# Kernel optimization log

Hardware: AMD Instinct MI355X
Metric: run time of the kernel (lower is better)

## Reference

```python
import jax, jax.numpy as jnp
import numpy as np

B, N = 256, 4096
IMG_W, IMG_H = 640.0, 480.0


def setup_inputs() -> dict:
    key = jax.random.key(0)
    k0, k1, k2, k3 = jax.random.split(key, 4)
    kpts0 = jax.random.uniform(k0, (B, N, 2), dtype=jnp.float32) * jnp.array([IMG_W, IMG_H], jnp.float32)
    kpts1 = jax.random.uniform(k1, (B, N, 2), dtype=jnp.float32) * jnp.array([IMG_W, IMG_H], jnp.float32)
    conf = jax.random.uniform(k2, (B, N, 1), dtype=jnp.float32)
    t_scale = jax.random.uniform(k3, (B, 2), dtype=jnp.float32) + 0.5
    Kmat = jnp.array([[500.0, 0.0, 320.0], [0.0, 500.0, 240.0], [0.0, 0.0, 1.0]], jnp.float32)
    K = jnp.tile(Kmat[None, None], (B, 2, 1, 1))
    gt_pose_0to1 = jnp.tile(jnp.eye(4, dtype=jnp.float32)[None], (B, 1, 1))
    return {"kpts0": kpts0, "kpts1": kpts1, "conf": conf, "t_scale": t_scale, "K": K, "gt_pose_0to1": gt_pose_0to1}


def _normalize(kpts, Kmat):
    # pixel -> normalized camera coords, homogeneous. kpts:[B,N,2], Kmat:[B,3,3] -> [B,N,3]
    Kinv = jnp.linalg.inv(Kmat)
    h = jnp.concatenate([kpts, jnp.ones_like(kpts[..., :1])], axis=-1)
    return jnp.einsum('bij,bnj->bni', Kinv, h)


def _se3_weighted_8pt(kpts0, kpts1, K0, K1, w, t_scale):
    b_, n_ = kpts0.shape[0], kpts0.shape[1]
    x0 = _normalize(kpts0, K0)  # [B,N,3]
    x1 = _normalize(kpts1, K1)  # [B,N,3]
    # epipolar constraint x1^T E x0 = 0 -> row kron(x1, x0): [B,N,9]
    X = (x1[..., :, None] * x0[..., None, :]).reshape(b_, n_, 9)
    # confidence-weighted normal equations, 9x9 per batch
    M = jnp.einsum('bn,bni,bnj->bij', w, X, X)
    _, V = jnp.linalg.eigh(M)
    E = V[..., 0].reshape(b_, 3, 3)  # eigvec of smallest eigenvalue
    # project to essential manifold + decompose
    U, S, Vt = jnp.linalg.svd(E)
    W = jnp.array([[0.0, -1.0, 0.0], [1.0, 0.0, 0.0], [0.0, 0.0, 1.0]], E.dtype)
    R1 = U @ W @ Vt
    R2 = U @ W.T @ Vt
    R1 = R1 * jnp.sign(jnp.linalg.det(R1))[:, None, None]
    R2 = R2 * jnp.sign(jnp.linalg.det(R2))[:, None, None]
    t = U[..., 2]  # [B,3]
    Rc = jnp.stack([R1, R1, R2, R2], axis=1)   # [B,4,3,3]
    tc = jnp.stack([t, -t, t, -t], axis=1)     # [B,4,3]
    # cheirality: solve d0 * (R x0) - d1 * x1 = -t in least squares (2x2 closed form)
    a = jnp.einsum('bcij,bnj->bcni', Rc, x0)   # [B,4,N,3]
    bvec = x1[:, None]                          # [B,1,N,3]
    tt = tc[:, :, None, :]                      # [B,4,1,3]
    aa = jnp.sum(a * a, -1)
    bb = jnp.sum(bvec * bvec, -1)
    ab = jnp.sum(a * bvec, -1)
    at = jnp.sum(a * tt, -1)
    bt = jnp.sum(bvec * tt, -1)
    det = aa * bb - ab * ab + 1e-9
    d0 = (-at * bb + ab * bt) / det
    d1 = (aa * bt - ab * at) / det
    pos = ((d0 > 0) & (d1 > 0)).astype(w.dtype)
    score = jnp.sum(w[:, None] * pos, -1)       # [B,4]
    best = jnp.argmax(jax.lax.stop_gradient(score), axis=-1)
    oh = jax.nn.one_hot(best, 4, dtype=kpts0.dtype)
    R = jnp.einsum('bc,bcij->bij', oh, Rc)
    t_best = jnp.einsum('bc,bci->bi', oh, tc)
    t_sc = t_best * t_scale[:, None]            # scale unit translation
    top = jnp.concatenate([R, t_sc[..., None]], axis=-1)  # [B,3,4]
    bot = jnp.broadcast_to(jnp.array([0.0, 0.0, 0.0, 1.0], R.dtype), (b_, 1, 4))
    return jnp.concatenate([top, bot], axis=1)  # [B,4,4]


def _se3_inverse(T):
    R = T[:, :3, :3]
    t = T[:, :3, 3:]
    Rt = jnp.swapaxes(R, -1, -2)
    tin = -(Rt @ t)
    top = jnp.concatenate([Rt, tin], axis=-1)
    bot = jnp.broadcast_to(jnp.array([0.0, 0.0, 0.0, 1.0], T.dtype), (T.shape[0], 1, 4))
    return jnp.concatenate([top, bot], axis=1)


def reference(kpts0, kpts1, conf, t_scale, K, gt_pose_0to1):
    w = conf[..., 0]
    T01 = _se3_weighted_8pt(kpts0, kpts1, K[:, 0], K[:, 1], w, t_scale[:, 0])
    T10 = _se3_inverse(T01)
    return jnp.stack([T01, T10], axis=1)  # [B,2,4,4]
```

## Files before the change

kernel.cpp:

```cpp
#include <hip/hip_runtime.h>
#include <math.h>

#define NBATCH 256
#define NPTS   4096

__device__ __forceinline__ void inv3x3d(const float* __restrict__ Km, double* Ki) {
  double a = Km[0], bb = Km[1], c = Km[2];
  double d = Km[3], e  = Km[4], f = Km[5];
  double g = Km[6], h  = Km[7], i = Km[8];
  double C00 =  e*i - f*h;
  double C01 = -(d*i - f*g);
  double C02 =  d*h - e*g;
  double det = a*C00 + bb*C01 + c*C02;
  double rd = 1.0/det;
  Ki[0] = C00*rd; Ki[1] = -(bb*i - c*h)*rd; Ki[2] =  (bb*f - c*e)*rd;
  Ki[3] = C01*rd; Ki[4] =  (a*i  - c*g)*rd; Ki[5] = -(a*f  - c*d)*rd;
  Ki[6] = C02*rd; Ki[7] = -(a*h - bb*g)*rd; Ki[8] =  (a*e  - bb*d)*rd;
}

#define IDX(r,c)   ((r)*((r)+1)/2+(c))
#define UPIDX(r,c) ((r)*9 - ((r)*((r)-1))/2 + ((c)-(r)))

#define K1_T   512
#define K1_PPT (NPTS / K1_T)

__global__ __launch_bounds__(K1_T, 2)
void k1_reduce(const float* __restrict__ kpts0,
               const float* __restrict__ kpts1,
               const float* __restrict__ conf,
               const float* __restrict__ Kmat,
               double* __restrict__ Mws)
{
  const int b    = blockIdx.x;
  const int tid  = threadIdx.x;
  const int lane = tid & 63;
  const int wv   = tid >> 6;

  __shared__ double red[K1_T/64][45];

  double Kd[9];
  float Ki0[9], Ki1[9];
  inv3x3d(Kmat + (size_t)b*18, Kd);
#pragma unroll
  for (int j=0;j<9;j++) Ki0[j] = (float)Kd[j];
  inv3x3d(Kmat + (size_t)b*18 + 9, Kd);
#pragma unroll
  for (int j=0;j<9;j++) Ki1[j] = (float)Kd[j];

  const float2* k0p = (const float2*)kpts0 + (size_t)b*NPTS;
  const float2* k1p = (const float2*)kpts1 + (size_t)b*NPTS;
  const float*  cp  = conf + (size_t)b*NPTS;

  float acc[45];
#pragma unroll
  for (int j=0;j<45;j++) acc[j] = 0.f;

  for (int p=0;p<K1_PPT;p++) {
    const int i = tid + p*K1_T;
    const float2 q0 = k0p[i];
    const float2 q1 = k1p[i];
    const float  w  = cp[i];
    float x0[3], x1[3];
    x0[0] = fmaf(Ki0[0],q0.x, fmaf(Ki0[1],q0.y, Ki0[2]));
    x0[1] = fmaf(Ki0[3],q0.x, fmaf(Ki0[4],q0.y, Ki0[5]));
    x0[2] = fmaf(Ki0[6],q0.x, fmaf(Ki0[7],q0.y, Ki0[8]));
    x1[0] = fmaf(Ki1[0],q1.x, fmaf(Ki1[1],q1.y, Ki1[2]));
    x1[1] = fmaf(Ki1[3],q1.x, fmaf(Ki1[4],q1.y, Ki1[5]));
    x1[2] = fmaf(Ki1[6],q1.x, fmaf(Ki1[7],q1.y, Ki1[8]));
    float X[9], wX[9];
#pragma unroll
    for (int ii=0; ii<3; ii++)
#pragma unroll
      for (int jj=0; jj<3; jj++)
        X[ii*3+jj] = x1[ii]*x0[jj];
#pragma unroll
    for (int j=0;j<9;j++) wX[j] = w*X[j];
    int k = 0;
#pragma unroll
    for (int r=0;r<9;r++)
#pragma unroll
      for (int c=r;c<9;c++) { acc[k] = fmaf(wX[r], X[c], acc[k]); k++; }
  }

#pragma unroll
  for (int j=0;j<45;j++) {
    float v = acc[j];
#pragma unroll
    for (int off=32; off>0; off>>=1) v += __shfl_xor(v, off, 64);
    acc[j] = v;
  }
  if (lane == 0) {
#pragma unroll
    for (int j=0;j<45;j++) red[wv][j] = (double)acc[j];
  }
  __syncthreads();
  if (tid < 45) {
    double s = 0.0;
#pragma unroll
    for (int wq=0; wq<K1_T/64; wq++) s += red[wq][tid];
    Mws[(size_t)b*45 + tid] = s;
  }
}

__global__ __launch_bounds__(64, 1)
void k2_solve(const double* __restrict__ Mws,
              float* __restrict__ Rws)
{
  const int b = blockIdx.x*64 + threadIdx.x;
  const double* Mb = Mws + (size_t)b*45;

  double L[45];
#pragma unroll
  for (int r=0;r<9;r++)
#pragma unroll
    for (int c=0;c<=r;c++)
      L[IDX(r,c)] = Mb[UPIDX(c,r)];

  double dinv[9];
#pragma unroll
  for (int k=0;k<9;k++) {
    double s = L[IDX(k,k)];
#pragma unroll
    for (int j=0;j<k;j++) s -= L[IDX(k,j)]*L[IDX(k,j)];
    double l = sqrt(fmax(s, 1e-30));
    L[IDX(k,k)] = l;
    dinv[k] = 1.0/l;
#pragma unroll
    for (int i2=k+1;i2<9;i2++) {
      double s2 = L[IDX(i2,k)];
#pragma unroll
      for (int j=0;j<k;j++) s2 -= L[IDX(i2,j)]*L[IDX(k,j)];
      L[IDX(i2,k)] = s2*dinv[k];
    }
  }

  double W[45];
#pragma unroll
  for (int j=0;j<9;j++) {
    W[IDX(j,j)] = dinv[j];
#pragma unroll
    for (int i2=j+1;i2<9;i2++) {
      double s = 0.0;
#pragma unroll
      for (int k=j;k<i2;k++) s += L[IDX(i2,k)]*W[IDX(k,j)];
      W[IDX(i2,j)] = -s*dinv[i2];
    }
  }

  double Bm[45];
#pragma unroll
  for (int i2=0;i2<9;i2++)
#pragma unroll
    for (int j=0;j<=i2;j++) {
      double s = 0.0;
#pragma unroll
      for (int k=i2;k<9;k++) s += W[IDX(k,i2)]*W[IDX(k,j)];
      Bm[IDX(i2,j)] = s;
    }

  double v[9];
#pragma unroll
  for (int j=0;j<9;j++) v[j] = 0.125;
  v[4] = 1.0;
  for (int it=0; it<20; it++) {
    double y[9];
#pragma unroll
    for (int i2=0;i2<9;i2++) {
      double s = 0.0;
#pragma unroll
      for (int j=0;j<9;j++) {
        const int rr = (i2>j)?i2:j, cc = (i2>j)?j:i2;
        s = fma(Bm[IDX(rr,cc)], v[j], s);
      }
      y[i2] = s;
    }
#pragma unroll
    for (int j=0;j<9;j++) v[j] = y[j];
  }
  {
    double nn = 0.0;
#pragma unroll
    for (int j=0;j<9;j++) nn += v[j]*v[j];
    double rn = 1.0/sqrt(nn);
#pragma unroll
    for (int j=0;j<9;j++) v[j] *= rn;
  }

  double E0[3][3];
#pragma unroll
  for (int ii=0;ii<3;ii++)
#pragma unroll
    for (int jj=0;jj<3;jj++) E0[ii][jj] = v[ii*3+jj];
  double G[3][3];
#pragma unroll
  for (int a2=0;a2<3;a2++)
#pragma unroll
    for (int b2=0;b2<3;b2++)
      G[a2][b2] = E0[0][a2]*E0[0][b2] + E0[1][a2]*E0[1][b2] + E0[2][a2]*E0[2][b2];
  double Vv[3][3] = {{1,0,0},{0,1,0},{0,0,1}};
#define JROT(P,Q,RR) do { \
    double apq = G[P][Q]; \
    if (fabs(apq) > 1e-300) { \
      double app = G[P][P], aqq = G[Q][Q]; \
      double tau = (aqq - app) / (2.0*apq); \
      double tt = ((tau >= 0.0) ? 1.0 : -1.0) / (fabs(tau) + sqrt(1.0 + tau*tau)); \
      double cc_ = 1.0/sqrt(1.0 + tt*tt); \
      double ss_ = tt*cc_; \
      G[P][P] = app - tt*apq; \
      G[Q][Q] = aqq + tt*apq; \
      G[P][Q] = 0.0; G[Q][P] = 0.0; \
      double grp = G[RR][P], grq = G[RR][Q]; \
      G[RR][P] = cc_*grp - ss_*grq; G[P][RR] = G[RR][P]; \
      G[RR][Q] = ss_*grp + cc_*grq; G[Q][RR] = G[RR][Q]; \
      double v0p = Vv[0][P], v0q = Vv[0][Q]; \
      Vv[0][P] = cc_*v0p - ss_*v0q; Vv[0][Q] = ss_*v0p + cc_*v0q; \
      double v1p = Vv[1][P], v1q = Vv[1][Q]; \
      Vv[1][P] = cc_*v1p - ss_*v1q; Vv[1][Q] = ss_*v1p + cc_*v1q; \
      double v2p = Vv[2][P], v2q = Vv[2][Q]; \
      Vv[2][P] = cc_*v2p - ss_*v2q; Vv[2][Q] = ss_*v2p + cc_*v2q; \
    } } while(0)
  for (int sw=0; sw<6; sw++) { JROT(0,1,2); JROT(0,2,1); JROT(1,2,0); }
#undef JROT
  double lam[3] = {G[0][0], G[1][1], G[2][2]};
#define CSWAP(A_,B_) if (lam[A_] < lam[B_]) { \
    double tl = lam[A_]; lam[A_] = lam[B_]; lam[B_] = tl; \
    double t0_ = Vv[0][A_]; Vv[0][A_] = Vv[0][B_]; Vv[0][B_] = t0_; \
    double t1_ = Vv[1][A_]; Vv[1][A_] = Vv[1][B_]; Vv[1][B_] = t1_; \
    double t2_ = Vv[2][A_]; Vv[2][A_] = Vv[2][B_]; Vv[2][B_] = t2_; }
  CSWAP(0,1); CSWAP(0,2); CSWAP(1,2);
#undef CSWAP
  double u1[3], u2[3], u3[3];
#pragma unroll
  for (int i3=0;i3<3;i3++)
    u1[i3] = E0[i3][0]*Vv[0][0] + E0[i3][1]*Vv[1][0] + E0[i3][2]*Vv[2][0];
  double n1 = 1.0/sqrt(fmax(u1[0]*u1[0]+u1[1]*u1[1]+u1[2]*u1[2], 1e-300));
#pragma unroll
  for (int i3=0;i3<3;i3++) u1[i3] *= n1;
#pragma unroll
  for (int i3=0;i3<3;i3++)
    u2[i3] = E0[i3][0]*Vv[0][1] + E0[i3][1]*Vv[1][1] + E0[i3][2]*Vv[2][1];
  double d12 = u1[0]*u2[0]+u1[1]*u2[1]+u1[2]*u2[2];
#pragma unroll
  for (int i3=0;i3<3;i3++) u2[i3] -= d12*u1[i3];
  double n2 = 1.0/sqrt(fmax(u2[0]*u2[0]+u2[1]*u2[1]+u2[2]*u2[2], 1e-300));
#pragma unroll
  for (int i3=0;i3<3;i3++) u2[i3] *= n2;
  u3[0] = u1[1]*u2[2] - u1[2]*u2[1];
  u3[1] = u1[2]*u2[0] - u1[0]*u2[2];
  u3[2] = u1[0]*u2[1] - u1[1]*u2[0];
  double R1a[9], R2a[9];
#pragma unroll
  for (int i3=0;i3<3;i3++)
#pragma unroll
    for (int j3=0;j3<3;j3++) {
      double m  = u3[i3]*Vv[j3][2];
      double pA = u2[i3]*Vv[j3][0] - u1[i3]*Vv[j3][1];
      R1a[i3*3+j3] = pA + m;
      R2a[i3*3+j3] = m - pA;
    }
  double det1 = R1a[0]*(R1a[4]*R1a[8]-R1a[5]*R1a[7])
              - R1a[1]*(R1a[3]*R1a[8]-R1a[5]*R1a[6])
              + R1a[2]*(R1a[3]*R1a[7]-R1a[4]*R1a[6]);
  double det2 = R2a[0]*(R2a[4]*R2a[8]-R2a[5]*R2a[7])
              - R2a[1]*(R2a[3]*R2a[8]-R2a[5]*R2a[6])
              + R2a[2]*(R2a[3]*R2a[7]-R2a[4]*R2a[6]);
  double sg1 = (det1 < 0.0) ? -1.0 : 1.0;
  double sg2 = (det2 < 0.0) ? -1.0 : 1.0;

  float* o = Rws + (size_t)b*21;
#pragma unroll
  for (int j=0;j<9;j++) { o[j] = (float)(sg1*R1a[j]); o[9+j] = (float)(sg2*R2a[j]); }
  o[18] = (float)u3[0]; o[19] = (float)u3[1]; o[20] = (float)u3[2];
}

#define K3_T   512
#define K3_PPT (NPTS / K3_T)

__global__ __launch_bounds__(K3_T, 2)
void k3_score(const float* __restrict__ kpts0,
              const float* __restrict__ kpts1,
              const float* __restrict__ conf,
              const float* __restrict__ t_scale,
              const float* __restrict__ Kmat,
              const float* __restrict__ Rws,
              float* __restrict__ out)
{
  const int b    = blockIdx.x;
  const int tid  = threadIdx.x;
  const int lane = tid & 63;
  const int wv   = tid >> 6;

  __shared__ float sscore[K3_T/64][4];

  double Kd[9];
  float Ki0[9], Ki1[9];
  inv3x3d(Kmat + (size_t)b*18, Kd);
#pragma unroll
  for (int j=0;j<9;j++) Ki0[j] = (float)Kd[j];
  inv3x3d(Kmat + (size_t)b*18 + 9, Kd);
#pragma unroll
  for (int j=0;j<9;j++) Ki1[j] = (float)Kd[j];

  const float* rb = Rws + (size_t)b*21;
  float r1[9], r2[9], tv[3];
#pragma unroll
  for (int j=0;j<9;j++) { r1[j] = rb[j]; r2[j] = rb[9+j]; }
  tv[0] = rb[18]; tv[1] = rb[19]; tv[2] = rb[20];

  const float2* k0p = (const float2*)kpts0 + (size_t)b*NPTS;
  const float2* k1p = (const float2*)kpts1 + (size_t)b*NPTS;
  const float*  cp  = conf + (size_t)b*NPTS;

  float sc[4] = {0.f, 0.f, 0.f, 0.f};
  for (int p=0;p<K3_PPT;p++) {
    const int i = tid + p*K3_T;
    const float2 q0 = k0p[i];
    const float2 q1 = k1p[i];
    const float  w  = cp[i];
    float x0[3], x1[3];
    x0[0] = fmaf(Ki0[0],q0.x, fmaf(Ki0[1],q0.y, Ki0[2]));
    x0[1] = fmaf(Ki0[3],q0.x, fmaf(Ki0[4],q0.y, Ki0[5]));
    x0[2] = fmaf(Ki0[6],q0.x, fmaf(Ki0[7],q0.y, Ki0[8]));
    x1[0] = fmaf(Ki1[0],q1.x, fmaf(Ki1[1],q1.y, Ki1[2]));
    x1[1] = fmaf(Ki1[3],q1.x, fmaf(Ki1[4],q1.y, Ki1[5]));
    x1[2] = fmaf(Ki1[6],q1.x, fmaf(Ki1[7],q1.y, Ki1[8]));
    const float bb2 = x1[0]*x1[0]+x1[1]*x1[1]+x1[2]*x1[2];
    const float bt  = x1[0]*tv[0]+x1[1]*tv[1]+x1[2]*tv[2];
    {
      float a0 = r1[0]*x0[0]+r1[1]*x0[1]+r1[2]*x0[2];
      float a1 = r1[3]*x0[0]+r1[4]*x0[1]+r1[5]*x0[2];
      float a2 = r1[6]*x0[0]+r1[7]*x0[1]+r1[8]*x0[2];
      float aa = a0*a0+a1*a1+a2*a2;
      float ab = a0*x1[0]+a1*x1[1]+a2*x1[2];
      float at = a0*tv[0]+a1*tv[1]+a2*tv[2];
      float n0v = ab*bt - at*bb2;
      float n1v = aa*bt - ab*at;
      if (n0v > 0.f && n1v > 0.f) sc[0] += w;
      if (n0v < 0.f && n1v < 0.f) sc[1] += w;
    }
    {
      float a0 = r2[0]*x0[0]+r2[1]*x0[1]+r2[2]*x0[2];
      float a1 = r2[3]*x0[0]+r2[4]*x0[1]+r2[5]*x0[2];
      float a2 = r2[6]*x0[0]+r2[7]*x0[1]+r2[8]*x0[2];
      float aa = a0*a0+a1*a1+a2*a2;
      float ab = a0*x1[0]+a1*x1[1]+a2*x1[2];
      float at = a0*tv[0]+a1*tv[1]+a2*tv[2];
      float n0v = ab*bt - at*bb2;
      float n1v = aa*bt - ab*at;
      if (n0v > 0.f && n1v > 0.f) sc[2] += w;
      if (n0v < 0.f && n1v < 0.f) sc[3] += w;
    }
  }
#pragma unroll
  for (int c=0;c<4;c++) {
    float vv = sc[c];
#pragma unroll
    for (int off=32; off>0; off>>=1) vv += __shfl_xor(vv, off, 64);
    sc[c] = vv;
  }
  if (lane == 0) {
#pragma unroll
    for (int c=0;c<4;c++) sscore[wv][c] = sc[c];
  }
  __syncthreads();

  if (tid == 0) {
    float st[4];
#pragma unroll
    for (int c=0;c<4;c++) {
      float s = 0.f;
#pragma unroll
      for (int wq=0; wq<K3_T/64; wq++) s += sscore[wq][c];
      st[c] = s;
    }
    int bestc = 0; float bs = st[0];
    if (st[1] > bs) { bs = st[1]; bestc = 1; }
    if (st[2] > bs) { bs = st[2]; bestc = 2; }
    if (st[3] > bs) { bs = st[3]; bestc = 3; }
    float Rb[9];
#pragma unroll
    for (int j=0;j<9;j++) Rb[j] = (bestc < 2) ? r1[j] : r2[j];
    const float sg = (bestc & 1) ? -1.f : 1.f;
    const float ts = t_scale[(size_t)b*2];
    const float t0 = sg*tv[0]*ts, t1 = sg*tv[1]*ts, t2 = sg*tv[2]*ts;
    float* o = out + (size_t)b*32;
    o[0]=Rb[0]; o[1]=Rb[1]; o[2] =Rb[2]; o[3] =t0;
    o[4]=Rb[3]; o[5]=Rb[4]; o[6] =Rb[5]; o[7] =t1;
    o[8]=Rb[6]; o[9]=Rb[7]; o[10]=Rb[8]; o[11]=t2;
    o[12]=0.f; o[13]=0.f; o[14]=0.f; o[15]=1.f;
    const float ti0 = -(Rb[0]*t0 + Rb[3]*t1 + Rb[6]*t2);
    const float ti1 = -(Rb[1]*t0 + Rb[4]*t1 + Rb[7]*t2);
    const float ti2 = -(Rb[2]*t0 + Rb[5]*t1 + Rb[8]*t2);
    o[16]=Rb[0]; o[17]=Rb[3]; o[18]=Rb[6]; o[19]=ti0;
    o[20]=Rb[1]; o[21]=Rb[4]; o[22]=Rb[7]; o[23]=ti1;
    o[24]=Rb[2]; o[25]=Rb[5]; o[26]=Rb[8]; o[27]=ti2;
    o[28]=0.f; o[29]=0.f; o[30]=0.f; o[31]=1.f;
  }
}

extern "C" void kernel_launch(void* const* d_in, const int* in_sizes, int n_in,
                              void* d_out, int out_size, void* d_ws, size_t ws_size,
                              hipStream_t stream) {
  (void)in_sizes; (void)n_in; (void)out_size; (void)ws_size;
  const float* kpts0  = (const float*)d_in[0];
  const float* kpts1  = (const float*)d_in[1];
  const float* conf   = (const float*)d_in[2];
  const float* tscale = (const float*)d_in[3];
  const float* K      = (const float*)d_in[4];
  float* outp = (float*)d_out;

  double* Mws = (double*)d_ws;
  float*  Rws = (float*)((char*)d_ws + (size_t)NBATCH*45*8);

  k1_reduce<<<dim3(NBATCH), dim3(K1_T), 0, stream>>>(kpts0, kpts1, conf, K, Mws);
  k2_solve <<<dim3(NBATCH/64), dim3(64), 0, stream>>>(Mws, Rws);
  k3_score <<<dim3(NBATCH), dim3(K3_T), 0, stream>>>(kpts0, kpts1, conf, tscale, K, Rws, outp);
}
```

Baseline: 101.8 us.

## Fuse reduction, eigen-solve and cheirality scoring into one per-batch kernel

Merges the three kernels into a single kernel with one block per batch. The 9x9 solve now runs on thread 0 of each block, with the normal-equation matrix and candidate poses passed through shared memory instead of global workspace. This removes two launches, the global round-trips, and the 4-block solve kernel that used only 256 threads. The cost is that 511 threads sit idle during a long serial double-precision solve in every block. Per-wave partials are also kept in float, and the in-place Cholesky inverse reuses L to save registers.

```diff
diff --git a/kernel.cpp b/kernel.cpp
--- a/kernel.cpp
+++ b/kernel.cpp
@@ -3,8 +3,14 @@
 
 #define NBATCH 256
 #define NPTS   4096
-
-__device__ __forceinline__ void inv3x3d(const float* __restrict__ Km, double* Ki) {
+#define NT     512
+#define PPT    (NPTS / NT)
+#define NWAVE  (NT / 64)
+
+#define IDX(r,c)   ((r)*((r)+1)/2+(c))
+#define UPIDX(r,c) ((r)*9 - ((r)*((r)-1))/2 + ((c)-(r)))
+
+__device__ __forceinline__ void inv3x3f(const float* __restrict__ Km, float* Ki) {
   double a = Km[0], bb = Km[1], c = Km[2];
   double d = Km[3], e  = Km[4], f = Km[5];
   double g = Km[6], h  = Km[7], i = Km[8];
@@ -13,39 +19,32 @@
   double C02 =  d*h - e*g;
   double det = a*C00 + bb*C01 + c*C02;
   double rd = 1.0/det;
-  Ki[0] = C00*rd; Ki[1] = -(bb*i - c*h)*rd; Ki[2] =  (bb*f - c*e)*rd;
-  Ki[3] = C01*rd; Ki[4] =  (a*i  - c*g)*rd; Ki[5] = -(a*f  - c*d)*rd;
-  Ki[6] = C02*rd; Ki[7] = -(a*h - bb*g)*rd; Ki[8] =  (a*e  - bb*d)*rd;
+  Ki[0] = (float)(C00*rd); Ki[1] = (float)(-(bb*i - c*h)*rd); Ki[2] = (float)( (bb*f - c*e)*rd);
+  Ki[3] = (float)(C01*rd); Ki[4] = (float)( (a*i  - c*g)*rd); Ki[5] = (float)(-(a*f  - c*d)*rd);
+  Ki[6] = (float)(C02*rd); Ki[7] = (float)(-(a*h - bb*g)*rd); Ki[8] = (float)( (a*e  - bb*d)*rd);
 }
 
-#define IDX(r,c)   ((r)*((r)+1)/2+(c))
-#define UPIDX(r,c) ((r)*9 - ((r)*((r)-1))/2 + ((c)-(r)))
-
-#define K1_T   512
-#define K1_PPT (NPTS / K1_T)
-
-__global__ __launch_bounds__(K1_T, 2)
-void k1_reduce(const float* __restrict__ kpts0,
-               const float* __restrict__ kpts1,
-               const float* __restrict__ conf,
-               const float* __restrict__ Kmat,
-               double* __restrict__ Mws)
+__global__ __launch_bounds__(NT, 1)
+void pose_fused(const float* __restrict__ kpts0,
+                const float* __restrict__ kpts1,
+                const float* __restrict__ conf,
+                const float* __restrict__ t_scale,
+                const float* __restrict__ Kmat,
+                float* __restrict__ out)
 {
   const int b    = blockIdx.x;
   const int tid  = threadIdx.x;
   const int lane = tid & 63;
   const int wv   = tid >> 6;
 
-  __shared__ double red[K1_T/64][45];
-
-  double Kd[9];
+  __shared__ float  red[NWAVE][45];
+  __shared__ double sMd[45];
+  __shared__ float  sR[21];
+  __shared__ float  sscore[NWAVE][4];
+
   float Ki0[9], Ki1[9];
-  inv3x3d(Kmat + (size_t)b*18, Kd);
-#pragma unroll
-  for (int j=0;j<9;j++) Ki0[j] = (float)Kd[j];
-  inv3x3d(Kmat + (size_t)b*18 + 9, Kd);
-#pragma unroll
-  for (int j=0;j<9;j++) Ki1[j] = (float)Kd[j];
+  inv3x3f(Kmat + (size_t)b*18,     Ki0);
+  inv3x3f(Kmat + (size_t)b*18 + 9, Ki1);
 
   const float2* k0p = (const float2*)kpts0 + (size_t)b*NPTS;
   const float2* k1p = (const float2*)kpts1 + (size_t)b*NPTS;
@@ -55,8 +54,9 @@
 #pragma unroll
   for (int j=0;j<45;j++) acc[j] = 0.f;
 
-  for (int p=0;p<K1_PPT;p++) {
-    const int i = tid + p*K1_T;
+#pragma unroll
+  for (int p=0;p<PPT;p++) {
+    const int i = tid + p*NT;
     const float2 q0 = k0p[i];
     const float2 q1 = k1p[i];
     const float  w  = cp[i];
@@ -91,229 +91,193 @@
   }
   if (lane == 0) {
 #pragma unroll
-    for (int j=0;j<45;j++) red[wv][j] = (double)acc[j];
+    for (int j=0;j<45;j++) red[wv][j] = acc[j];
   }
   __syncthreads();
   if (tid < 45) {
     double s = 0.0;
 #pragma unroll
-    for (int wq=0; wq<K1_T/64; wq++) s += red[wq][tid];
-    Mws[(size_t)b*45 + tid] = s;
-  }
-}
-
-__global__ __launch_bounds__(64, 1)
-void k2_solve(const double* __restrict__ Mws,
-              float* __restrict__ Rws)
-{
-  const int b = blockIdx.x*64 + threadIdx.x;
-  const double* Mb = Mws + (size_t)b*45;
-
-  double L[45];
-#pragma unroll
-  for (int r=0;r<9;r++)
-#pragma unroll
-    for (int c=0;c<=r;c++)
-      L[IDX(r,c)] = Mb[UPIDX(c,r)];
-
-  double dinv[9];
-#pragma unroll
-  for (int k=0;k<9;k++) {
-    double s = L[IDX(k,k)];
-#pragma unroll
-    for (int j=0;j<k;j++) s -= L[IDX(k,j)]*L[IDX(k,j)];
-    double l = sqrt(fmax(s, 1e-30));
-    L[IDX(k,k)] = l;
-    dinv[k] = 1.0/l;
-#pragma unroll
-    for (int i2=k+1;i2<9;i2++) {
-      double s2 = L[IDX(i2,k)];
-#pragma unroll
-      for (int j=0;j<k;j++) s2 -= L[IDX(i2,j)]*L[IDX(k,j)];
-      L[IDX(i2,k)] = s2*dinv[k];
-    }
-  }
-
-  double W[45];
-#pragma unroll
-  for (int j=0;j<9;j++) {
-    W[IDX(j,j)] = dinv[j];
-#pragma unroll
-    for (int i2=j+1;i2<9;i2++) {
-      double s = 0.0;
-#pragma unroll
-      for (int k=j;k<i2;k++) s += L[IDX(i2,k)]*W[IDX(k,j)];
-      W[IDX(i2,j)] = -s*dinv[i2];
-    }
-  }
-
-  double Bm[45];
-#pragma unroll
-  for (int i2=0;i2<9;i2++)
-#pragma unroll
-    for (int j=0;j<=i2;j++) {
-      double s = 0.0;
-#pragma unroll
-      for (int k=i2;k<9;k++) s += W[IDX(k,i2)]*W[IDX(k,j)];
-      Bm[IDX(i2,j)] = s;
-    }
-
-  double v[9];
-#pragma unroll
-  for (int j=0;j<9;j++) v[j] = 0.125;
-  v[4] = 1.0;
-  for (int it=0; it<20; it++) {
-    double y[9];
+    for (int wq=0; wq<NWAVE; wq++) s += (double)red[wq][tid];
+    sMd[tid] = s;
+  }
+  __syncthreads();
+
+  if (tid == 0) {
+    double L[45];
+#pragma unroll
+    for (int r=0;r<9;r++)
+#pragma unroll
+      for (int c=0;c<=r;c++)
+        L[IDX(r,c)] = sMd[UPIDX(c,r)];
+
+    double dinv[9];
+#pragma unroll
+    for (int k=0;k<9;k++) {
+      double s = L[IDX(k,k)];
+#pragma unroll
+      for (int j=0;j<k;j++) s -= L[IDX(k,j)]*L[IDX(k,j)];
+      double l = sqrt(fmax(s, 1e-30));
+      L[IDX(k,k)] = l;
+      dinv[k] = 1.0/l;
+#pragma unroll
+      for (int i2=k+1;i2<9;i2++) {
+        double s2 = L[IDX(i2,k)];
+#pragma unroll
+        for (int j=0;j<k;j++) s2 -= L[IDX(i2,j)]*L[IDX(k,j)];
+        L[IDX(i2,k)] = s2*dinv[k];
+      }
+    }
+
+#pragma unroll
+    for (int j=0;j<9;j++) {
+#pragma unroll
+      for (int i2=j+1;i2<9;i2++) {
+        double s = L[IDX(i2,j)]*dinv[j];
+#pragma unroll
+        for (int k=j+1;k<i2;k++) s += L[IDX(i2,k)]*L[IDX(k,j)];
+        L[IDX(i2,j)] = -s*dinv[i2];
+      }
+    }
+#pragma unroll
+    for (int j=0;j<9;j++) L[IDX(j,j)] = dinv[j];
+
 #pragma unroll
     for (int i2=0;i2<9;i2++) {
-      double s = 0.0;
-#pragma unroll
-      for (int j=0;j<9;j++) {
-        const int rr = (i2>j)?i2:j, cc = (i2>j)?j:i2;
-        s = fma(Bm[IDX(rr,cc)], v[j], s);
-      }
-      y[i2] = s;
-    }
-#pragma unroll
-    for (int j=0;j<9;j++) v[j] = y[j];
-  }
-  {
-    double nn = 0.0;
-#pragma unroll
-    for (int j=0;j<9;j++) nn += v[j]*v[j];
-    double rn = 1.0/sqrt(nn);
-#pragma unroll
-    for (int j=0;j<9;j++) v[j] *= rn;
-  }
-
-  double E0[3][3];
-#pragma unroll
-  for (int ii=0;ii<3;ii++)
-#pragma unroll
-    for (int jj=0;jj<3;jj++) E0[ii][jj] = v[ii*3+jj];
-  double G[3][3];
-#pragma unroll
-  for (int a2=0;a2<3;a2++)
-#pragma unroll
-    for (int b2=0;b2<3;b2++)
-      G[a2][b2] = E0[0][a2]*E0[0][b2] + E0[1][a2]*E0[1][b2] + E0[2][a2]*E0[2][b2];
-  double Vv[3][3] = {{1,0,0},{0,1,0},{0,0,1}};
+      double tmp[9];
+#pragma unroll
+      for (int j=0;j<=i2;j++) {
+        double s = 0.0;
+#pragma unroll
+        for (int k=i2;k<9;k++) s += L[IDX(k,i2)]*L[IDX(k,j)];
+        tmp[j] = s;
+      }
+#pragma unroll
+      for (int j=0;j<=i2;j++) L[IDX(i2,j)] = tmp[j];
+    }
+
+    double v[9];
+#pragma unroll
+    for (int j=0;j<9;j++) v[j] = 0.125;
+    v[4] = 1.0;
+    for (int it=0; it<20; it++) {
+      double y[9];
+#pragma unroll
+      for (int i2=0;i2<9;i2++) {
+        double s = 0.0;
+#pragma unroll
+        for (int j=0;j<9;j++) {
+          const int rr = (i2>j)?i2:j, cc = (i2>j)?j:i2;
+          s = fma(L[IDX(rr,cc)], v[j], s);
+        }
+        y[i2] = s;
+      }
+#pragma unroll
+      for (int j=0;j<9;j++) v[j] = y[j];
+    }
+    {
+      double nn = 0.0;
+#pragma unroll
+      for (int j=0;j<9;j++) nn += v[j]*v[j];
+      double rn = 1.0/sqrt(nn);
+#pragma unroll
+      for (int j=0;j<9;j++) v[j] *= rn;
+    }
+
+    double E0[3][3];
+#pragma unroll
+    for (int ii=0;ii<3;ii++)
+#pragma unroll
+      for (int jj=0;jj<3;jj++) E0[ii][jj] = v[ii*3+jj];
+    double G[3][3];
+#pragma unroll
+    for (int a2=0;a2<3;a2++)
+#pragma unroll
+      for (int b2=0;b2<3;b2++)
+        G[a2][b2] = E0[0][a2]*E0[0][b2] + E0[1][a2]*E0[1][b2] + E0[2][a2]*E0[2][b2];
+    double Vv[3][3] = {{1,0,0},{0,1,0},{0,0,1}};
 #define JROT(P,Q,RR) do { \
-    double apq = G[P][Q]; \
-    if (fabs(apq) > 1e-300) { \
-      double app = G[P][P], aqq = G[Q][Q]; \
-      double tau = (aqq - app) / (2.0*apq); \
-      double tt = ((tau >= 0.0) ? 1.0 : -1.0) / (fabs(tau) + sqrt(1.0 + tau*tau)); \
-      double cc_ = 1.0/sqrt(1.0 + tt*tt); \
-      double ss_ = tt*cc_; \
-      G[P][P] = app - tt*apq; \
-      G[Q][Q] = aqq + tt*apq; \
-      G[P][Q] = 0.0; G[Q][P] = 0.0; \
-      double grp = G[RR][P], grq = G[RR][Q]; \
-      G[RR][P] = cc_*grp - ss_*grq; G[P][RR] = G[RR][P]; \
-      G[RR][Q] = ss_*grp + cc_*grq; G[Q][RR] = G[RR][Q]; \
-      double v0p = Vv[0][P], v0q = Vv[0][Q]; \
-      Vv[0][P] = cc_*v0p - ss_*v0q; Vv[0][Q] = ss_*v0p + cc_*v0q; \
-      double v1p = Vv[1][P], v1q = Vv[1][Q]; \
-      Vv[1][P] = cc_*v1p - ss_*v1q; Vv[1][Q] = ss_*v1p + cc_*v1q; \
-      double v2p = Vv[2][P], v2q = Vv[2][Q]; \
-      Vv[2][P] = cc_*v2p - ss_*v2q; Vv[2][Q] = ss_*v2p + cc_*v2q; \
-    } } while(0)
-  for (int sw=0; sw<6; sw++) { JROT(0,1,2); JROT(0,2,1); JROT(1,2,0); }
+      double apq = G[P][Q]; \
+      if (fabs(apq) > 1e-300) { \
+        double app = G[P][P], aqq = G[Q][Q]; \
+        double tau = (aqq - app) / (2.0*apq); \
+        double tt = ((tau >= 0.0) ? 1.0 : -1.0) / (fabs(tau) + sqrt(1.0 + tau*tau)); \
+        double cc_ = 1.0/sqrt(1.0 + tt*tt); \
+        double ss_ = tt*cc_; \
+        G[P][P] = app - tt*apq; \
+        G[Q][Q] = aqq + tt*apq; \
+        G[P][Q] = 0.0; G[Q][P] = 0.0; \
+        double grp = G[RR][P], grq = G[RR][Q]; \
+        G[RR][P] = cc_*grp - ss_*grq; G[P][RR] = G[RR][P]; \
+        G[RR][Q] = ss_*grp + cc_*grq; G[Q][RR] = G[RR][Q]; \
+        double v0p = Vv[0][P], v0q = Vv[0][Q]; \
+        Vv[0][P] = cc_*v0p - ss_*v0q; Vv[0][Q] = ss_*v0p + cc_*v0q; \
+        double v1p = Vv[1][P], v1q = Vv[1][Q]; \
+        Vv[1][P] = cc_*v1p - ss_*v1q; Vv[1][Q] = ss_*v1p + cc_*v1q; \
+        double v2p = Vv[2][P], v2q = Vv[2][Q]; \
+        Vv[2][P] = cc_*v2p - ss_*v2q; Vv[2][Q] = ss_*v2p + cc_*v2q; \
+      } } while(0)
+    for (int sw=0; sw<6; sw++) { JROT(0,1,2); JROT(0,2,1); JROT(1,2,0); }
 #undef JROT
-  double lam[3] = {G[0][0], G[1][1], G[2][2]};
+    double lam[3] = {G[0][0], G[1][1], G[2][2]};
 #define CSWAP(A_,B_) if (lam[A_] < lam[B_]) { \
-    double tl = lam[A_]; lam[A_] = lam[B_]; lam[B_] = tl; \
-    double t0_ = Vv[0][A_]; Vv[0][A_] = Vv[0][B_]; Vv[0][B_] = t0_; \
-    double t1_ = Vv[1][A_]; Vv[1][A_] = Vv[1][B_]; Vv[1][B_] = t1_; \
-    double t2_ = Vv[2][A_]; Vv[2][A_] = Vv[2][B_]; Vv[2][B_] = t2_; }
-  CSWAP(0,1); CSWAP(0,2); CSWAP(1,2);
+      double tl = lam[A_]; lam[A_] = lam[B_]; lam[B_] = tl; \
+      double t0_ = Vv[0][A_]; Vv[0][A_] = Vv[0][B_]; Vv[0][B_] = t0_; \
+      double t1_ = Vv[1][A_]; Vv[1][A_] = Vv[1][B_]; Vv[1][B_] = t1_; \
+      double t2_ = Vv[2][A_]; Vv[2][A_] = Vv[2][B_]; Vv[2][B_] = t2_; }
+    CSWAP(0,1); CSWAP(0,2); CSWAP(1,2);
 #undef CSWAP
-  double u1[3], u2[3], u3[3];
-#pragma unroll
-  for (int i3=0;i3<3;i3++)
-    u1[i3] = E0[i3][0]*Vv[0][0] + E0[i3][1]*Vv[1][0] + E0[i3][2]*Vv[2][0];
-  double n1 = 1.0/sqrt(fmax(u1[0]*u1[0]+u1[1]*u1[1]+u1[2]*u1[2], 1e-300));
-#pragma unroll
-  for (int i3=0;i3<3;i3++) u1[i3] *= n1;
-#pragma unroll
-  for (int i3=0;i3<3;i3++)
-    u2[i3] = E0[i3][0]*Vv[0][1] + E0[i3][1]*Vv[1][1] + E0[i3][2]*Vv[2][1];
-  double d12 = u1[0]*u2[0]+u1[1]*u2[1]+u1[2]*u2[2];
-#pragma unroll
-  for (int i3=0;i3<3;i3++) u2[i3] -= d12*u1[i3];
-  double n2 = 1.0/sqrt(fmax(u2[0]*u2[0]+u2[1]*u2[1]+u2[2]*u2[2], 1e-300));
-#pragma unroll
-  for (int i3=0;i3<3;i3++) u2[i3] *= n2;
-  u3[0] = u1[1]*u2[2] - u1[2]*u2[1];
-  u3[1] = u1[2]*u2[0] - u1[0]*u2[2];
-  u3[2] = u1[0]*u2[1] - u1[1]*u2[0];
-  double R1a[9], R2a[9];
-#pragma unroll
-  for (int i3=0;i3<3;i3++)
-#pragma unroll
-    for (int j3=0;j3<3;j3++) {
-      double m  = u3[i3]*Vv[j3][2];
-      double pA = u2[i3]*Vv[j3][0] - u1[i3]*Vv[j3][1];
-      R1a[i3*3+j3] = pA + m;
-      R2a[i3*3+j3] = m - pA;
-    }
-  double det1 = R1a[0]*(R1a[4]*R1a[8]-R1a[5]*R1a[7])
-              - R1a[1]*(R1a[3]*R1a[8]-R1a[5]*R1a[6])
-              + R1a[2]*(R1a[3]*R1a[7]-R1a[4]*R1a[6]);
-  double det2 = R2a[0]*(R2a[4]*R2a[8]-R2a[5]*R2a[7])
-              - R2a[1]*(R2a[3]*R2a[8]-R2a[5]*R2a[6])
-              + R2a[2]*(R2a[3]*R2a[7]-R2a[4]*R2a[6]);
-  double sg1 = (det1 < 0.0) ? -1.0 : 1.0;
-  double sg2 = (det2 < 0.0) ? -1.0 : 1.0;
-
-  float* o = Rws + (size_t)b*21;
-#pragma unroll
-  for (int j=0;j<9;j++) { o[j] = (float)(sg1*R1a[j]); o[9+j] = (float)(sg2*R2a[j]); }
-  o[18] = (float)u3[0]; o[19] = (float)u3[1]; o[20] = (float)u3[2];
-}
-
-#define K3_T   512
-#define K3_PPT (NPTS / K3_T)
-
-__global__ __launch_bounds__(K3_T, 2)
-void k3_score(const float* __restrict__ kpts0,
-              const float* __restrict__ kpts1,
-              const float* __restrict__ conf,
-              const float* __restrict__ t_scale,
-              const float* __restrict__ Kmat,
-              const float* __restrict__ Rws,
-              float* __restrict__ out)
-{
-  const int b    = blockIdx.x;
-  const int tid  = threadIdx.x;
-  const int lane = tid & 63;
-  const int wv   = tid >> 6;
-
-  __shared__ float sscore[K3_T/64][4];
-
-  double Kd[9];
-  float Ki0[9], Ki1[9];
-  inv3x3d(Kmat + (size_t)b*18, Kd);
-#pragma unroll
-  for (int j=0;j<9;j++) Ki0[j] = (float)Kd[j];
-  inv3x3d(Kmat + (size_t)b*18 + 9, Kd);
-#pragma unroll
-  for (int j=0;j<9;j++) Ki1[j] = (float)Kd[j];
-
-  const float* rb = Rws + (size_t)b*21;
+    double u1[3], u2[3], u3[3];
+#pragma unroll
+    for (int i3=0;i3<3;i3++)
+      u1[i3] = E0[i3][0]*Vv[0][0] + E0[i3][1]*Vv[1][0] + E0[i3][2]*Vv[2][0];
+    double n1 = 1.0/sqrt(fmax(u1[0]*u1[0]+u1[1]*u1[1]+u1[2]*u1[2], 1e-300));
+#pragma unroll
+    for (int i3=0;i3<3;i3++) u1[i3] *= n1;
+#pragma unroll
+    for (int i3=0;i3<3;i3++)
+      u2[i3] = E0[i3][0]*Vv[0][1] + E0[i3][1]*Vv[1][1] + E0[i3][2]*Vv[2][1];
+    double d12 = u1[0]*u2[0]+u1[1]*u2[1]+u1[2]*u2[2];
+#pragma unroll
+    for (int i3=0;i3<3;i3++) u2[i3] -= d12*u1[i3];
+    double n2 = 1.0/sqrt(fmax(u2[0]*u2[0]+u2[1]*u2[1]+u2[2]*u2[2], 1e-300));
+#pragma unroll
+    for (int i3=0;i3<3;i3++) u2[i3] *= n2;
+    u3[0] = u1[1]*u2[2] - u1[2]*u2[1];
+    u3[1] = u1[2]*u2[0] - u1[0]*u2[2];
+    u3[2] = u1[0]*u2[1] - u1[1]*u2[0];
+    double R1a[9], R2a[9];
+#pragma unroll
+    for (int i3=0;i3<3;i3++)
+#pragma unroll
+      for (int j3=0;j3<3;j3++) {
+        double m  = u3[i3]*Vv[j3][2];
+        double pA = u2[i3]*Vv[j3][0] - u1[i3]*Vv[j3][1];
+        R1a[i3*3+j3] = pA + m;
+        R2a[i3*3+j3] = m - pA;
+      }
+    double det1 = R1a[0]*(R1a[4]*R1a[8]-R1a[5]*R1a[7])
+                - R1a[1]*(R1a[3]*R1a[8]-R1a[5]*R1a[6])
+                + R1a[2]*(R1a[3]*R1a[7]-R1a[4]*R1a[6]);
+    double det2 = R2a[0]*(R2a[4]*R2a[8]-R2a[5]*R2a[7])
+                - R2a[1]*(R2a[3]*R2a[8]-R2a[5]*R2a[6])
+                + R2a[2]*(R2a[3]*R2a[7]-R2a[4]*R2a[6]);
+    double sg1 = (det1 < 0.0) ? -1.0 : 1.0;
+    double sg2 = (det2 < 0.0) ? -1.0 : 1.0;
+#pragma unroll
+    for (int j3=0;j3<9;j3++) { sR[j3] = (float)(sg1*R1a[j3]); sR[9+j3] = (float)(sg2*R2a[j3]); }
+    sR[18] = (float)u3[0]; sR[19] = (float)u3[1]; sR[20] = (float)u3[2];
+  }
+  __syncthreads();
+
   float r1[9], r2[9], tv[3];
 #pragma unroll
-  for (int j=0;j<9;j++) { r1[j] = rb[j]; r2[j] = rb[9+j]; }
-  tv[0] = rb[18]; tv[1] = rb[19]; tv[2] = rb[20];
-
-  const float2* k0p = (const float2*)kpts0 + (size_t)b*NPTS;
-  const float2* k1p = (const float2*)kpts1 + (size_t)b*NPTS;
-  const float*  cp  = conf + (size_t)b*NPTS;
+  for (int j=0;j<9;j++) { r1[j] = sR[j]; r2[j] = sR[9+j]; }
+  tv[0] = sR[18]; tv[1] = sR[19]; tv[2] = sR[20];
 
   float sc[4] = {0.f, 0.f, 0.f, 0.f};
-  for (int p=0;p<K3_PPT;p++) {
-    const int i = tid + p*K3_T;
+#pragma unroll
+  for (int p=0;p<PPT;p++) {
+    const int i = tid + p*NT;
     const float2 q0 = k0p[i];
     const float2 q1 = k1p[i];
     const float  w  = cp[i];
@@ -370,7 +334,7 @@
     for (int c=0;c<4;c++) {
       float s = 0.f;
 #pragma unroll
-      for (int wq=0; wq<K3_T/64; wq++) s += sscore[wq][c];
+      for (int wq=0; wq<NWAVE; wq++) s += sscore[wq][c];
       st[c] = s;
     }
     int bestc = 0; float bs = st[0];
@@ -401,18 +365,12 @@
 extern "C" void kernel_launch(void* const* d_in, const int* in_sizes, int n_in,
                               void* d_out, int out_size, void* d_ws, size_t ws_size,
                               hipStream_t stream) {
-  (void)in_sizes; (void)n_in; (void)out_size; (void)ws_size;
+  (void)in_sizes; (void)n_in; (void)out_size; (void)d_ws; (void)ws_size;
   const float* kpts0  = (const float*)d_in[0];
   const float* kpts1  = (const float*)d_in[1];
   const float* conf   = (const float*)d_in[2];
   const float* tscale = (const float*)d_in[3];
   const float* K      = (const float*)d_in[4];
   float* outp = (float*)d_out;
-
-  double* Mws = (double*)d_ws;
-  float*  Rws = (float*)((char*)d_ws + (size_t)NBATCH*45*8);
-
-  k1_reduce<<<dim3(NBATCH), dim3(K1_T), 0, stream>>>(kpts0, kpts1, conf, K, Mws);
-  k2_solve <<<dim3(NBATCH/64), dim3(64), 0, stream>>>(Mws, Rws);
-  k3_score <<<dim3(NBATCH), dim3(K3_T), 0, stream>>>(kpts0, kpts1, conf, tscale, K, Rws, outp);
+  pose_fused<<<dim3(NBATCH), dim3(NT), 0, stream>>>(kpts0, kpts1, conf, tscale, K, outp);
 }
```

Result: faster. 98.23 us (-3.5%).
